# Optimization experiments

Hardware: AMD Instinct MI355X
Metric: run time of the kernel (lower is better)

## Reference

```python
import jax, jax.numpy as jnp
import numpy as np

B, S, D = 8, 8192, 1024
FILTER_SIZE = 4


def setup_inputs() -> dict:
    key = jax.random.key(0)
    k1, k2, k3 = jax.random.split(key, 3)
    x = jax.random.normal(k1, (B, S, D), dtype=jnp.float32)
    # projection to [bias, filter_size coefficients]
    W = jax.random.normal(k2, (D, FILTER_SIZE + 1), dtype=jnp.float32) / np.sqrt(D)
    noise = jax.random.uniform(k3, (B, S, 1), dtype=jnp.float32)
    return {"x": x, "W": W, "noise": noise}


def reference(x, W, noise):
    """Sequentially-dependent gater.
    gate_logits[i] = log p(g_i=1 | g_{<i}), gate_probs[i] = p, gate_samples[i] ~ Bernoulli(p).
    Filter weights are a linear projection of x; the per-step logit is
    bias + <coeffs, last filter_size samples> (zeros before t=0).
    Returns (gate_logits, gate_probs, gate_samples), each [B, S, 1].
    """
    b, s, d = x.shape
    fsz = W.shape[1] - 1
    # precompute_filter_weights: [B, S, 1+filter_size]
    fw = jnp.einsum('bsd,df->bsf', x, W)

    def step(window, inputs):
        # window: [B, fsz] most recent samples, oldest first
        fw_t, u_t = inputs  # [B, 1+fsz], [B]
        logit = fw_t[:, 0] + jnp.sum(window * fw_t[:, 1:], axis=-1)  # [B]
        logp = jax.nn.log_sigmoid(logit)
        p = jax.nn.sigmoid(logit)
        samp = (u_t < p).astype(x.dtype)
        new_window = jnp.concatenate([window[:, 1:], samp[:, None]], axis=1)
        return new_window, (logp, p, samp)

    window0 = jnp.zeros((b, fsz), dtype=x.dtype)
    xs = (jnp.swapaxes(fw, 0, 1), jnp.swapaxes(noise[..., 0], 0, 1))  # [S, B, ...]
    _, (logps, ps, samps) = jax.lax.scan(step, window0, xs)

    to_out = lambda a: jnp.swapaxes(a, 0, 1)[..., None]  # [S,B] -> [B,S,1]
    return to_out(logps), to_out(ps), to_out(samps)
```

## Files before the change

kernel.cpp:

```cpp
#include <hip/hip_runtime.h>
#include <cstdint>
#include <cstddef>


namespace {

constexpr int kB = 8;
constexpr int kS = 8192;
constexpr int kD = 1024;
constexpr int kRows = kB * kS;
constexpr int kT = 64;
constexpr int kCPB = kS / kT;
constexpr int kChunks = kB * kCPB;
constexpr unsigned long long kIdMap = 0xFEDCBA9876543210ull;

__device__ __forceinline__ float logit_from_state(unsigned int w,
                                                  const float4& A,
                                                  const float4& Bv) {
  const float s1 = (w & 1u) ? A.y : 0.0f;
  const float s2 = (w & 2u) ? A.z : 0.0f;
  const float s3 = (w & 4u) ? A.w : 0.0f;
  const float s4 = (w & 8u) ? Bv.x : 0.0f;
  return A.x + (((s1 + s2) + s3) + s4);
}

__device__ __forceinline__ unsigned long long compose(unsigned long long a,
                                                      unsigned long long b) {
  unsigned long long r = 0;
#pragma unroll
  for (int s = 0; s < 16; ++s) {
    const unsigned int e = (unsigned int)(a >> (4 * s)) & 15u;
    r |= ((b >> (4 * e)) & 15ull) << (4 * s);
  }
  return r;
}

}

__global__ __launch_bounds__(256, 2) void proj_map_kernel(
    const float* __restrict__ x, const float* __restrict__ W,
    const float* __restrict__ noise, float* __restrict__ fwu,
    unsigned long long* __restrict__ trajbuf,
    unsigned long long* __restrict__ maps) {
  __shared__ float Wl[kD * 5];
  __shared__ float fl[kT * 8];
  const int tid = threadIdx.x;

  const float4* W4 = reinterpret_cast<const float4*>(W);
  float4* Wl4 = reinterpret_cast<float4*>(Wl);
#pragma unroll
  for (int i = 0; i < 5; ++i) Wl4[tid + 256 * i] = W4[tid + 256 * i];
  __syncthreads();

  const int lane = tid & 63;
  const int wv = tid >> 6;
  const int chunk = blockIdx.x;
  const int r0 = chunk * kT;
  const int rw0 = r0 + wv * 16;

  float wr[4][4][5];
#pragma unroll
  for (int j = 0; j < 4; ++j)
#pragma unroll
    for (int k = 0; k < 4; ++k) {
      const int d = j * 256 + lane * 4 + k;
#pragma unroll
      for (int f = 0; f < 5; ++f) wr[j][k][f] = Wl[d * 5 + f];
    }

  float nu = 0.5f, nth = 0.0f;
  if (lane < 16) {
    nu = noise[rw0 + lane];
    nth = logf(nu / (1.0f - nu));
  }

  auto pref = [&](float4(&v)[4], int t) {
    if (t < 16) {
      const float4* xp =
          reinterpret_cast<const float4*>(x + (size_t)(rw0 + t) * kD);
#pragma unroll
      for (int j = 0; j < 4; ++j) v[j] = xp[j * 64 + lane];
    }
  };

  auto do_row = [&](const float4(&v)[4], int t) {
    float acc[5] = {0.f, 0.f, 0.f, 0.f, 0.f};
#pragma unroll
    for (int j = 0; j < 4; ++j) {
      const float e[4] = {v[j].x, v[j].y, v[j].z, v[j].w};
#pragma unroll
      for (int k = 0; k < 4; ++k)
#pragma unroll
        for (int f = 0; f < 5; ++f) acc[f] += e[k] * wr[j][k][f];
    }
#pragma unroll
    for (int off = 32; off >= 1; off >>= 1)
#pragma unroll
      for (int f = 0; f < 5; ++f) acc[f] += __shfl_xor(acc[f], off);

    const float u = __shfl(nu, t);
    const float th = __shfl(nth, t);
    if (lane == 0) {
      const int row = rw0 + t;
      const float4 o0 = make_float4(acc[0], acc[1], acc[2], acc[3]);
      const float4 o1 = make_float4(acc[4], u, th, 0.0f);
      float4* og = reinterpret_cast<float4*>(fwu + (size_t)row * 8);
      og[0] = o0;
      og[1] = o1;
      float4* ol = reinterpret_cast<float4*>(&fl[(wv * 16 + t) * 8]);
      ol[0] = o0;
      ol[1] = o1;
    }
  };

  float4 va[4], vb[4];
  pref(va, 0);
  pref(vb, 1);
#pragma unroll 1
  for (int tp = 0; tp < 8; ++tp) {
    do_row(va, 2 * tp);
    pref(va, 2 * tp + 2);
    do_row(vb, 2 * tp + 1);
    pref(vb, 2 * tp + 3);
  }
  __syncthreads();

  if (wv == 0) {
    unsigned int cur = (unsigned int)(lane & 15);
    unsigned long long traj = 0;
#pragma unroll 8
    for (int i = 0; i < kT; ++i) {
      const float4* p = reinterpret_cast<const float4*>(&fl[i * 8]);
      const float4 A = p[0];
      const float4 Bv = p[1];
      const unsigned int d = (logit_from_state(cur, A, Bv) > Bv.z) ? 1u : 0u;
      traj |= (unsigned long long)d << i;
      cur = (cur >> 1) | (d << 3);
    }
    if (lane < 16) trajbuf[(size_t)chunk * 16 + lane] = traj;
    const unsigned long long b0 = __ballot((int)(cur & 1u));
    const unsigned long long b1 = __ballot((int)(cur & 2u));
    const unsigned long long b2 = __ballot((int)(cur & 4u));
    const unsigned long long b3 = __ballot((int)(cur & 8u));
    if (lane == 0) {
      unsigned long long m = 0;
#pragma unroll
      for (int s = 0; s < 16; ++s) {
        const unsigned long long e =
            ((b0 >> s) & 1ull) | (((b1 >> s) & 1ull) << 1) |
            (((b2 >> s) & 1ull) << 2) | (((b3 >> s) & 1ull) << 3);
        m |= e << (4 * s);
      }
      maps[chunk] = m;
    }
  }
}

__global__ __launch_bounds__(256) void scan_emit_kernel(
    const float* __restrict__ fwu, const unsigned long long* __restrict__ maps,
    const unsigned long long* __restrict__ trajbuf, float* __restrict__ out) {
  __shared__ unsigned int starts_lds[kCPB];
  const int tid = threadIdx.x;
  const int lane = tid & 63;
  const int wv = tid >> 6;
  const int c0 = blockIdx.x * 4;
  const int b = c0 / kCPB;
  const int chunk = c0 + wv;
  const int row = chunk * kT + lane;

  const float4* p = reinterpret_cast<const float4*>(fwu + (size_t)row * 8);
  const float4 A = p[0];
  const float4 Bv = p[1];
  unsigned long long tj = 0;
  if (lane < 16) tj = trajbuf[(size_t)chunk * 16 + lane];

  if (wv == 0) {
    const int L = lane;
    const unsigned long long m0 = maps[b * kCPB + 2 * L];
    const unsigned long long m1 = maps[b * kCPB + 2 * L + 1];
    unsigned long long scan = compose(m0, m1);
#pragma unroll
    for (int off = 1; off < 64; off <<= 1) {
      const unsigned long long prev = __shfl_up(scan, off);
      if (L >= off) scan = compose(prev, scan);
    }
    unsigned long long pref = __shfl_up(scan, 1);
    if (L == 0) pref = kIdMap;
    const unsigned int s0 = (unsigned int)(pref & 15ull);
    starts_lds[2 * L] = s0;
    starts_lds[2 * L + 1] = (unsigned int)((m0 >> (4 * s0)) & 15ull);
  }
  __syncthreads();

  const unsigned int st = starts_lds[chunk & (kCPB - 1)];
  const unsigned long long traj = __shfl(tj, (int)st);

  unsigned int w;
  if (lane >= 4)
    w = (unsigned int)(traj >> (lane - 4)) & 15u;
  else
    w = ((st >> lane) | ((unsigned int)traj << (4 - lane))) & 15u;

  const float logit = logit_from_state(w, A, Bv);
  const float pr = 1.0f / (1.0f + expf(-logit));
  const float lp = fminf(logit, 0.0f) - log1pf(expf(-fabsf(logit)));
  out[row] = lp;
  out[kRows + row] = pr;
  out[2 * kRows + row] = (float)((traj >> lane) & 1ull);
}

extern "C" void kernel_launch(void* const* d_in, const int* in_sizes, int n_in,
                              void* d_out, int out_size, void* d_ws,
                              size_t ws_size, hipStream_t stream) {
  const float* x = (const float*)d_in[0];
  const float* W = (const float*)d_in[1];
  const float* noise = (const float*)d_in[2];
  float* out = (float*)d_out;

  float* fwu = (float*)d_ws;
  unsigned long long* trajbuf =
      (unsigned long long*)((char*)d_ws + (size_t)kRows * 8 * sizeof(float));
  unsigned long long* maps =
      (unsigned long long*)((char*)trajbuf +
                            (size_t)kChunks * 16 * sizeof(unsigned long long));

  proj_map_kernel<<<kChunks, 256, 0, stream>>>(x, W, noise, fwu, trajbuf, maps);
  scan_emit_kernel<<<kChunks / 4, 256, 0, stream>>>(fwu, maps, trajbuf, out);
}
```

Baseline: 60.85 us.

## Shrink scan chunks to 16 rows, simulate per-wave, give each wave 32 rows

```diff
diff --git a/kernel.cpp b/kernel.cpp
--- a/kernel.cpp
+++ b/kernel.cpp
@@ -9,9 +9,10 @@
 constexpr int kS = 8192;
 constexpr int kD = 1024;
 constexpr int kRows = kB * kS;
-constexpr int kT = 64;
+constexpr int kT = 16;
 constexpr int kCPB = kS / kT;
 constexpr int kChunks = kB * kCPB;
+constexpr int kRPW = 32;
 constexpr unsigned long long kIdMap = 0xFEDCBA9876543210ull;
 
 __device__ __forceinline__ float logit_from_state(unsigned int w,
@@ -40,23 +41,25 @@
 __global__ __launch_bounds__(256, 2) void proj_map_kernel(
     const float* __restrict__ x, const float* __restrict__ W,
     const float* __restrict__ noise, float* __restrict__ fwu,
-    unsigned long long* __restrict__ trajbuf,
-    unsigned long long* __restrict__ maps) {
+    unsigned int* __restrict__ trajbuf, unsigned long long* __restrict__ maps) {
   __shared__ float Wl[kD * 5];
-  __shared__ float fl[kT * 8];
+  __shared__ float fl[4][kT * 8];
   const int tid = threadIdx.x;
+  const int lane = tid & 63;
+  const int wv = tid >> 6;
+  const int wid = blockIdx.x * 4 + wv;
+  const int r0 = wid * kRPW;
+
+  float nu = 0.5f, nth = 0.0f;
+  if (lane < kRPW) nu = noise[r0 + lane];
 
   const float4* W4 = reinterpret_cast<const float4*>(W);
   float4* Wl4 = reinterpret_cast<float4*>(Wl);
 #pragma unroll
   for (int i = 0; i < 5; ++i) Wl4[tid + 256 * i] = W4[tid + 256 * i];
+
+  if (lane < kRPW) nth = logf(nu / (1.0f - nu));
   __syncthreads();
-
-  const int lane = tid & 63;
-  const int wv = tid >> 6;
-  const int chunk = blockIdx.x;
-  const int r0 = chunk * kT;
-  const int rw0 = r0 + wv * 16;
 
   float wr[4][4][5];
 #pragma unroll
@@ -68,16 +71,10 @@
       for (int f = 0; f < 5; ++f) wr[j][k][f] = Wl[d * 5 + f];
     }
 
-  float nu = 0.5f, nth = 0.0f;
-  if (lane < 16) {
-    nu = noise[rw0 + lane];
-    nth = logf(nu / (1.0f - nu));
-  }
-
-  auto pref = [&](float4(&v)[4], int t) {
-    if (t < 16) {
+  auto prefetch_row = [&](float4(&v)[4], int t) {
+    if (t < kRPW) {
       const float4* xp =
-          reinterpret_cast<const float4*>(x + (size_t)(rw0 + t) * kD);
+          reinterpret_cast<const float4*>(x + (size_t)(r0 + t) * kD);
 #pragma unroll
       for (int j = 0; j < 4; ++j) v[j] = xp[j * 64 + lane];
     }
@@ -101,43 +98,30 @@
     const float u = __shfl(nu, t);
     const float th = __shfl(nth, t);
     if (lane == 0) {
-      const int row = rw0 + t;
       const float4 o0 = make_float4(acc[0], acc[1], acc[2], acc[3]);
       const float4 o1 = make_float4(acc[4], u, th, 0.0f);
-      float4* og = reinterpret_cast<float4*>(fwu + (size_t)row * 8);
+      float4* og = reinterpret_cast<float4*>(fwu + (size_t)(r0 + t) * 8);
       og[0] = o0;
       og[1] = o1;
-      float4* ol = reinterpret_cast<float4*>(&fl[(wv * 16 + t) * 8]);
+      float4* ol = reinterpret_cast<float4*>(&fl[wv][(t & 15) * 8]);
       ol[0] = o0;
       ol[1] = o1;
     }
   };
 
-  float4 va[4], vb[4];
-  pref(va, 0);
-  pref(vb, 1);
-#pragma unroll 1
-  for (int tp = 0; tp < 8; ++tp) {
-    do_row(va, 2 * tp);
-    pref(va, 2 * tp + 2);
-    do_row(vb, 2 * tp + 1);
-    pref(vb, 2 * tp + 3);
-  }
-  __syncthreads();
-
-  if (wv == 0) {
+  auto sim = [&](int c) {
     unsigned int cur = (unsigned int)(lane & 15);
-    unsigned long long traj = 0;
-#pragma unroll 8
+    unsigned int traj = 0;
+#pragma unroll
     for (int i = 0; i < kT; ++i) {
-      const float4* p = reinterpret_cast<const float4*>(&fl[i * 8]);
+      const float4* p = reinterpret_cast<const float4*>(&fl[wv][i * 8]);
       const float4 A = p[0];
       const float4 Bv = p[1];
       const unsigned int d = (logit_from_state(cur, A, Bv) > Bv.z) ? 1u : 0u;
-      traj |= (unsigned long long)d << i;
+      traj |= d << i;
       cur = (cur >> 1) | (d << 3);
     }
-    if (lane < 16) trajbuf[(size_t)chunk * 16 + lane] = traj;
+    if (lane < 16) trajbuf[(size_t)c * 16 + lane] = traj;
     const unsigned long long b0 = __ballot((int)(cur & 1u));
     const unsigned long long b1 = __ballot((int)(cur & 2u));
     const unsigned long long b2 = __ballot((int)(cur & 4u));
@@ -151,62 +135,81 @@
             (((b2 >> s) & 1ull) << 2) | (((b3 >> s) & 1ull) << 3);
         m |= e << (4 * s);
       }
-      maps[chunk] = m;
-    }
+      maps[c] = m;
+    }
+  };
+
+  float4 va[4], vb[4];
+  prefetch_row(va, 0);
+  prefetch_row(vb, 1);
+#pragma unroll 1
+  for (int tp = 0; tp < 16; ++tp) {
+    do_row(va, 2 * tp);
+    prefetch_row(va, 2 * tp + 2);
+    do_row(vb, 2 * tp + 1);
+    prefetch_row(vb, 2 * tp + 3);
+    if (tp == 7) sim(wid * 2);
+    if (tp == 15) sim(wid * 2 + 1);
   }
 }
 
 __global__ __launch_bounds__(256) void scan_emit_kernel(
     const float* __restrict__ fwu, const unsigned long long* __restrict__ maps,
-    const unsigned long long* __restrict__ trajbuf, float* __restrict__ out) {
-  __shared__ unsigned int starts_lds[kCPB];
+    const unsigned int* __restrict__ trajbuf, float* __restrict__ out) {
+  __shared__ unsigned char starts_lds[kCPB];
   const int tid = threadIdx.x;
   const int lane = tid & 63;
   const int wv = tid >> 6;
-  const int c0 = blockIdx.x * 4;
-  const int b = c0 / kCPB;
-  const int chunk = c0 + wv;
-  const int row = chunk * kT + lane;
+  const int bid = blockIdx.x;
+  const int b = bid >> 5;
+  const int row = bid * 256 + tid;
 
   const float4* p = reinterpret_cast<const float4*>(fwu + (size_t)row * 8);
   const float4 A = p[0];
   const float4 Bv = p[1];
-  unsigned long long tj = 0;
-  if (lane < 16) tj = trajbuf[(size_t)chunk * 16 + lane];
 
   if (wv == 0) {
-    const int L = lane;
-    const unsigned long long m0 = maps[b * kCPB + 2 * L];
-    const unsigned long long m1 = maps[b * kCPB + 2 * L + 1];
-    unsigned long long scan = compose(m0, m1);
+    unsigned long long m[8];
+    const unsigned long long* mb = maps + b * kCPB + lane * 8;
+#pragma unroll
+    for (int i = 0; i < 8; ++i) m[i] = mb[i];
+    unsigned long long c = m[0];
+#pragma unroll
+    for (int i = 1; i < 8; ++i) c = compose(c, m[i]);
+    unsigned long long scan = c;
 #pragma unroll
     for (int off = 1; off < 64; off <<= 1) {
       const unsigned long long prev = __shfl_up(scan, off);
-      if (L >= off) scan = compose(prev, scan);
+      if (lane >= off) scan = compose(prev, scan);
     }
     unsigned long long pref = __shfl_up(scan, 1);
-    if (L == 0) pref = kIdMap;
-    const unsigned int s0 = (unsigned int)(pref & 15ull);
-    starts_lds[2 * L] = s0;
-    starts_lds[2 * L + 1] = (unsigned int)((m0 >> (4 * s0)) & 15ull);
+    if (lane == 0) pref = kIdMap;
+    unsigned int s = (unsigned int)(pref & 15ull);
+#pragma unroll
+    for (int i = 0; i < 8; ++i) {
+      starts_lds[lane * 8 + i] = (unsigned char)s;
+      s = (unsigned int)((m[i] >> (4 * s)) & 15ull);
+    }
   }
   __syncthreads();
 
-  const unsigned int st = starts_lds[chunk & (kCPB - 1)];
-  const unsigned long long traj = __shfl(tj, (int)st);
-
+  const int scl = (row & (kS - 1)) >> 4;
+  const int scg = row >> 4;
+  const unsigned int st = (unsigned int)starts_lds[scl];
+  const unsigned int traj = trajbuf[(size_t)scg * 16 + st];
+  const int i = row & 15;
   unsigned int w;
-  if (lane >= 4)
-    w = (unsigned int)(traj >> (lane - 4)) & 15u;
+  if (i >= 4)
+    w = (traj >> (i - 4)) & 15u;
   else
-    w = ((st >> lane) | ((unsigned int)traj << (4 - lane))) & 15u;
+    w = ((st >> i) | (traj << (4 - i))) & 15u;
 
   const float logit = logit_from_state(w, A, Bv);
   const float pr = 1.0f / (1.0f + expf(-logit));
   const float lp = fminf(logit, 0.0f) - log1pf(expf(-fabsf(logit)));
   out[row] = lp;
   out[kRows + row] = pr;
-  out[2 * kRows + row] = (float)((traj >> lane) & 1ull);
+  out[2 * kRows + row] = (float)((traj >> i) & 1u);
 }
 
 extern "C" void kernel_launch(void* const* d_in, const int* in_sizes, int n_in,
@@ -218,12 +221,12 @@
   float* out = (float*)d_out;
 
   float* fwu = (float*)d_ws;
-  unsigned long long* trajbuf =
-      (unsigned long long*)((char*)d_ws + (size_t)kRows * 8 * sizeof(float));
+  unsigned int* trajbuf =
+      (unsigned int*)((char*)d_ws + (size_t)kRows * 8 * sizeof(float));
   unsigned long long* maps =
       (unsigned long long*)((char*)trajbuf +
-                            (size_t)kChunks * 16 * sizeof(unsigned long long));
-
-  proj_map_kernel<<<kChunks, 256, 0, stream>>>(x, W, noise, fwu, trajbuf, maps);
-  scan_emit_kernel<<<kChunks / 4, 256, 0, stream>>>(fwu, maps, trajbuf, out);
-}
+                            (size_t)kChunks * 16 * sizeof(unsigned int));
+
+  proj_map_kernel<<<512, 256, 0, stream>>>(x, W, noise, fwu, trajbuf, maps);
+  scan_emit_kernel<<<kRows / 256, 256, 0, stream>>>(fwu, maps, trajbuf, out);
+}
```

New measurement: 55.19 us, median of 2. 1.1x faster.
